# Performance work log

Hardware: AMD Instinct MI355X
Metric: run time of the kernel (lower is better)

Reference implementation:

```python
import jax, jax.numpy as jnp
import numpy as np

N = 50000
E = 800000
IN_F = 256
ATT_D = 256
H = 8
D_K = ATT_D // H  # 32
NORM_IDX = 0  # opt['attention_norm_idx']


def setup_inputs() -> dict:
    key = jax.random.key(0)
    ks = jax.random.split(key, 10)
    x = jax.random.normal(ks[0], (N, IN_F), dtype=jnp.float32)
    edge = jax.random.randint(ks[1], (2, E), 0, N, dtype=jnp.int64)
    edge_weights = jax.random.uniform(ks[2], (E,), dtype=jnp.float32)
    s = 0.02
    Wq = jax.random.normal(ks[3], (ATT_D, IN_F), dtype=jnp.float32) * s
    bq = jax.random.normal(ks[4], (ATT_D,), dtype=jnp.float32) * s
    Wk = jax.random.normal(ks[5], (ATT_D, IN_F), dtype=jnp.float32) * s
    bk = jax.random.normal(ks[6], (ATT_D,), dtype=jnp.float32) * s
    Wv = jax.random.normal(ks[7], (ATT_D, IN_F), dtype=jnp.float32) * s
    bv = jax.random.normal(ks[8], (ATT_D,), dtype=jnp.float32) * s
    return {"x": x, "edge": edge, "edge_weights": edge_weights,
            "Wq": Wq, "bq": bq, "Wk": Wk, "bk": bk, "Wv": Wv, "bv": bv}


def _segment_softmax(logits, seg, num_segments):
    # scatter-softmax grouped by seg (torch_geometric.utils.softmax semantics)
    m = jax.ops.segment_max(logits, seg, num_segments=num_segments)  # [N, H]
    ex = jnp.exp(logits - m[seg])
    s = jax.ops.segment_sum(ex, seg, num_segments=num_segments)
    return ex / (s[seg] + 1e-16)


def reference(x, edge, edge_weights, Wq, bq, Wk, bk, Wv, bv):
    # Linear projections, then [N, H, D_K] -> transpose to [N, D_K, H]
    q = (x @ Wq.T + bq).reshape(N, H, D_K).transpose(0, 2, 1)
    k = (x @ Wk.T + bk).reshape(N, H, D_K).transpose(0, 2, 1)
    v = (x @ Wv.T + bv).reshape(N, H, D_K).transpose(0, 2, 1)
    src = q[edge[0]]      # [E, D_K, H]
    dst_k = k[edge[1]]    # [E, D_K, H]
    prods = jnp.sum(src * dst_k, axis=1) / np.sqrt(D_K)  # [E, H]
    prods = prods * edge_weights[:, None]
    attention = _segment_softmax(prods, edge[NORM_IDX], N)  # [E, H]
    return attention, v
```

## Files before the change

kernel.cpp:

```cpp
#include <hip/hip_runtime.h>

#define NN 50000
#define EE 800000
#define FF 256
#define HH 8
#define DK 32

typedef short bf16x8 __attribute__((ext_vector_type(8)));
typedef float f32x4  __attribute__((ext_vector_type(4)));

__device__ __forceinline__ float b2f(short s) {
    return __uint_as_float(((unsigned)(unsigned short)s) << 16);
}
__device__ __forceinline__ short f2b(float f) {
    unsigned u = __float_as_uint(f);
    return (short)((u + 0x7fff + ((u >> 16) & 1)) >> 16);
}

__device__ __forceinline__ void gld16(void* lds, const void* g) {
    __builtin_amdgcn_global_load_lds(
        (const __attribute__((address_space(1))) unsigned int*)g,
        (__attribute__((address_space(3))) unsigned int*)lds,
        16, 0, 0);
}

__global__ __launch_bounds__(256) void sniff_all(
    const void* x, const void* ew, const void* wq, const void* bq,
    const void* wk, const void* bk, const void* wv, const void* bv,
    const void* edge, int* __restrict__ flags)
{
    __shared__ int tot;
    if (threadIdx.x == 0) tot = 0;
    __syncthreads();
    int b = blockIdx.x;
    if (b < 8) {
        const void* ptrs[8] = {x, ew, wq, bq, wk, bk, wv, bv};
        const int   ns[8]   = {NN * FF, EE, FF * FF, FF, FF * FF, FF, FF * FF, FF};
        const unsigned short* p = (const unsigned short*)ptrs[b];
        int half = ns[b] >> 1;
        int S = half < 4096 ? half : 4096;
        int cnt = 0;
        for (int i = threadIdx.x; i < S; i += 256) {
            unsigned v = p[2 * i];
            cnt += (((v >> 7) & 0xFF) >= 0xC0) ? 1 : 0;
        }
        atomicAdd(&tot, cnt);
        __syncthreads();
        if (threadIdx.x == 0) flags[b] = (tot * 32 > S) ? 1 : 0;
    } else {
        const unsigned* e32 = (const unsigned*)edge;
        int cnt = 0;
        for (int i = threadIdx.x; i < 4096; i += 256)
            cnt += (e32[2 * i + 1] != 0u) ? 1 : 0;
        atomicAdd(&tot, cnt);
        __syncthreads();
        if (threadIdx.x == 0) flags[8] = (tot < 100) ? 1 : 0;
    }
}

__global__ __launch_bounds__(256) void convert_wb(
    const void* wq, const void* wk, const void* wv,
    const void* bq, const void* bk, const void* bv,
    short* __restrict__ wb, float* __restrict__ bb,
    const int* __restrict__ flags)
{
    int b = blockIdx.x;
    if (b < 96) {
        int mat = b >> 5;
        const void* src = mat == 0 ? wq : mat == 1 ? wk : wv;
        int isf = flags[2 + mat * 2];
        int base = (b & 31) * 2048 + threadIdx.x * 8;
        bf16x8 v;
        if (isf) {
            const f32x4* pp = (const f32x4*)((const float*)src + base);
            f32x4 a = pp[0], c = pp[1];
            #pragma unroll
            for (int j = 0; j < 4; ++j) { v[j] = f2b(a[j]); v[4 + j] = f2b(c[j]); }
        } else {
            v = *(const bf16x8*)((const short*)src + base);
        }
        int row = base >> 8, k = base & 255;
        int s = k >> 5, quad = (k >> 3) & 3;
        int pc = (row << 2) + (quad ^ ((row >> 1) & 3));
        *(bf16x8*)(wb + mat * (FF * FF) + s * 8192 + pc * 8) = v;
    } else {
        #pragma unroll
        for (int mat = 0; mat < 3; ++mat) {
            const void* src = mat == 0 ? bq : mat == 1 ? bk : bv;
            int isf = flags[3 + mat * 2];
            int i = threadIdx.x;
            bb[mat * FF + i] = isf ? ((const float*)src)[i]
                                   : b2f(((const short*)src)[i]);
        }
    }
}

__global__ __launch_bounds__(256) void qkv_gemm(
    const void* __restrict__ x, const short* __restrict__ wb,
    const float* __restrict__ bb, short* __restrict__ qo,
    short* __restrict__ ko, float* __restrict__ vo,
    const int* __restrict__ flags, int ybase)
{
    __shared__ __align__(16) short wlds[2][8192];
    const int isf32x = flags[0];
    const int tid = threadIdx.x, wave = tid >> 6, lane = tid & 63;
    const int l16 = lane & 15, quad = lane >> 4;
    const int mat = ybase + blockIdx.y;
    const short* W = wb + mat * (FF * FF);
    const int rows0 = blockIdx.x * 64 + wave * 16;
    const int rowa = rows0 + l16;
    const int rowc = rowa < NN ? rowa : NN - 1;
    const int koff = quad * 8;
    const size_t xrow = (size_t)rowc * FF;

    const int rdo = l16 * 32 + ((quad ^ ((l16 >> 1) & 3)) << 3);

    f32x4 acc[16] = {};
    f32x4 ar0[2], ar1[2];
    bf16x8 ab[2];

    #define STAGE(buf, s) do {                                                  \
        const short* gs_ = W + (s) * 8192;                                      \
        _Pragma("unroll")                                                       \
        for (int i_ = 0; i_ < 4; ++i_)                                          \
            gld16(&wlds[buf][(i_ * 256 + (tid & ~63)) * 8],                     \
                  gs_ + (size_t)(i_ * 256 + tid) * 8);                          \
    } while (0)

    #define ALOAD(slot, s) do {                                                 \
        if (isf32x) {                                                           \
            const f32x4* p_ = (const f32x4*)((const float*)x + xrow + (s) * 32 + koff); \
            ar0[slot] = p_[0]; ar1[slot] = p_[1];                               \
        } else {                                                                \
            ab[slot] = *(const bf16x8*)((const short*)x + xrow + (s) * 32 + koff); \
        }                                                                       \
    } while (0)

    STAGE(0, 0);
    ALOAD(0, 0);
    __syncthreads();

    #pragma unroll
    for (int s = 0; s < 8; ++s) {
        const int cur = s & 1;
        if (s < 7) { STAGE(cur ^ 1, s + 1); ALOAD((s + 1) & 1, s + 1); }
        bf16x8 a;
        if (isf32x) {
            #pragma unroll
            for (int j = 0; j < 4; ++j) { a[j] = f2b(ar0[cur][j]); a[4 + j] = f2b(ar1[cur][j]); }
        } else {
            a = ab[cur];
        }
        const short* ws0 = &wlds[cur][rdo];
        #pragma unroll
        for (int c = 0; c < 16; ++c) {
            bf16x8 bf = *(const bf16x8*)(ws0 + c * 512);
            acc[c] = __builtin_amdgcn_mfma_f32_16x16x32_bf16(a, bf, acc[c], 0, 0, 0);
        }
        __syncthreads();
    }

    const float* bias = bb + mat * FF;
    short* slice = (short*)wlds + wave * 4096;

    if (mat == 2) {
        float* lsf = (float*)slice;
        #pragma unroll
        for (int h = 0; h < 2; ++h) {
            #pragma unroll
            for (int ci = 0; ci < 8; ++ci) {
                int c = ci * 2 + h;
                int col = c * 16 + l16;
                float bv = bias[col];
                int pcl = l16 * 8 + ci;
                #pragma unroll
                for (int rr = 0; rr < 4; ++rr)
                    lsf[(quad * 4 + rr) * 128 + pcl] = acc[c][rr] + bv;
            }
            #pragma unroll
            for (int it = 0; it < 8; ++it) {
                int idx = it * 64 + lane;
                int r = idx >> 5, cc = idx & 31;
                int row = rows0 + r;
                if (row < NN)
                    *(f32x4*)(vo + (size_t)row * FF + h * 128 + cc * 4) =
                        ((const f32x4*)lsf)[idx];
            }
        }
    } else {
        #pragma unroll
        for (int c = 0; c < 16; ++c) {
            int col = c * 16 + l16;
            float bv = bias[col];
            #pragma unroll
            for (int rr = 0; rr < 4; ++rr)
                slice[(quad * 4 + rr) * 256 + col] = f2b(acc[c][rr] + bv);
        }
        short* out = (mat == 0) ? qo : ko;
        #pragma unroll
        for (int it = 0; it < 8; ++it) {
            int idx = it * 64 + lane;
            int r = idx >> 5, cc = idx & 31;
            int row = rows0 + r;
            if (row < NN)
                *(bf16x8*)(out + (size_t)row * FF + cc * 8) =
                    *(const bf16x8*)(slice + r * 256 + cc * 8);
        }
    }
}

__device__ __forceinline__ float edge_exp_f(
    const int* __restrict__ edge, const void* __restrict__ ew,
    const short* __restrict__ q, const short* __restrict__ k,
    int t, int isf32, int is64, int* s_out)
{
    int e = t >> 3, h = t & 7;
    int s = is64 ? edge[2 * (size_t)e] : edge[e];
    int d = is64 ? edge[2 * ((size_t)EE + e)] : edge[EE + e];
    *s_out = s;
    const short* qp = q + (size_t)s * FF + h * DK;
    const short* kp = k + (size_t)d * FF + h * DK;
    float dot = 0.f;
    #pragma unroll
    for (int i = 0; i < 4; ++i) {
        bf16x8 qa = *(const bf16x8*)(qp + i * 8);
        bf16x8 ka = *(const bf16x8*)(kp + i * 8);
        #pragma unroll
        for (int j = 0; j < 8; ++j) dot += b2f(qa[j]) * b2f(ka[j]);
    }
    float w = isf32 ? ((const float*)ew)[e] : b2f(((const short*)ew)[e]);
    return __expf(dot * 0.17677669529663687f * w);
}

__global__ __launch_bounds__(256) void edge_pass_a(
    const int* __restrict__ edge, const void* __restrict__ ew,
    const short* __restrict__ q, const short* __restrict__ k,
    float* __restrict__ sums, float* __restrict__ expbuf,
    const int* __restrict__ flags, int use_exp)
{
    int t = blockIdx.x * 256 + threadIdx.x;
    int s;
    float exv = edge_exp_f(edge, ew, q, k, t, flags[1], flags[8], &s);
    if (use_exp) expbuf[t] = exv;
    atomicAdd(&sums[s * HH + (threadIdx.x & 7)], exv);
}

__global__ __launch_bounds__(256) void edge_pass_b(
    const int* __restrict__ edge, const void* __restrict__ ew,
    const short* __restrict__ q, const short* __restrict__ k,
    const float* __restrict__ sums, const float* __restrict__ expbuf,
    float* __restrict__ att, const int* __restrict__ flags, int use_exp)
{
    int t = blockIdx.x * 256 + threadIdx.x;
    float exv; int s;
    if (use_exp) {
        int e = t >> 3;
        s = flags[8] ? edge[2 * (size_t)e] : edge[e];
        exv = expbuf[t];
    } else {
        exv = edge_exp_f(edge, ew, q, k, t, flags[1], flags[8], &s);
    }
    att[t] = exv / (sums[s * HH + (t & 7)] + 1e-16f);
}

extern "C" void kernel_launch(void* const* d_in, const int* in_sizes, int n_in,
                              void* d_out, int out_size, void* d_ws, size_t ws_size,
                              hipStream_t stream) {
    const void* x    = d_in[0];
    const int*  edge = (const int*)d_in[1];
    const void* ew   = d_in[2];
    const void* Wq   = d_in[3];
    const void* bq   = d_in[4];
    const void* Wk   = d_in[5];
    const void* bk   = d_in[6];
    const void* Wv   = d_in[7];
    const void* bv   = d_in[8];

    float* att_out = (float*)d_out;
    float* v_out   = att_out + (size_t)EE * HH;

    char*  ws    = (char*)d_ws;
    int*   flags = (int*)ws;
    float* sums  = (float*)(ws + 256);
    const size_t SUMS_B = (size_t)NN * HH * 4;
    const size_t Q_B    = (size_t)NN * FF * 2;
    short* q_  = (short*)(ws + 256 + SUMS_B);
    short* wb  = (short*)(ws + 256 + SUMS_B + Q_B);
    float* bb  = (float*)(ws + 256 + SUMS_B + Q_B + 3 * FF * FF * 2);
    float* expb = (float*)(ws + 256 + SUMS_B + Q_B + 3 * FF * FF * 2 + 3 * FF * 4);
    const size_t BASE_B = 256 + SUMS_B + Q_B + 3 * FF * FF * 2 + 3 * FF * 4;
    const int use_exp = (ws_size >= BASE_B + (size_t)EE * HH * 4) ? 1 : 0;

    short* k_ = (short*)v_out;

    sniff_all<<<9, 256, 0, stream>>>(x, ew, Wq, bq, Wk, bk, Wv, bv, edge, flags);
    convert_wb<<<97, 256, 0, stream>>>(Wq, Wk, Wv, bq, bk, bv, wb, bb, flags);
    hipMemsetAsync(sums, 0, SUMS_B, stream);

    dim3 gqk((NN + 63) / 64, 2);
    qkv_gemm<<<gqk, 256, 0, stream>>>(x, wb, bb, q_, k_, nullptr, flags, 0);

    const int nEH = EE * HH;
    edge_pass_a<<<nEH / 256, 256, 0, stream>>>(edge, ew, q_, k_, sums, expb, flags, use_exp);
    edge_pass_b<<<nEH / 256, 256, 0, stream>>>(edge, ew, q_, k_, sums, expb, att_out, flags, use_exp);

    dim3 gv((NN + 63) / 64, 1);
    qkv_gemm<<<gv, 256, 0, stream>>>(x, wb, bb, nullptr, nullptr, v_out, flags, 2);
}
```

Measured before the change: 321.8 us.

## Fuse Q/K/V projections into one GEMM pass and precompute reciprocal softmax sums

The QKV GEMM now loads each block's x rows into registers once and loops over the weight matrices inside a single launch. It computes all three projections in one kernel when workspace allows, storing K in workspace instead of aliasing the V output. This removes the repeated x reads and the separate V GEMM launch, at the cost of more register pressure and less grid parallelism per launch. A small kernel also inverts the per-node softmax sums so the normalisation pass multiplies instead of divides, which adds one extra launch.

```diff
diff --git a/kernel.cpp b/kernel.cpp
--- a/kernel.cpp
+++ b/kernel.cpp
@@ -99,14 +99,12 @@
     const void* __restrict__ x, const short* __restrict__ wb,
     const float* __restrict__ bb, short* __restrict__ qo,
     short* __restrict__ ko, float* __restrict__ vo,
-    const int* __restrict__ flags, int ybase)
+    const int* __restrict__ flags, int mlo, int mhi)
 {
     __shared__ __align__(16) short wlds[2][8192];
     const int isf32x = flags[0];
     const int tid = threadIdx.x, wave = tid >> 6, lane = tid & 63;
     const int l16 = lane & 15, quad = lane >> 4;
-    const int mat = ybase + blockIdx.y;
-    const short* W = wb + mat * (FF * FF);
     const int rows0 = blockIdx.x * 64 + wave * 16;
     const int rowa = rows0 + l16;
     const int rowc = rowa < NN ? rowa : NN - 1;
@@ -115,98 +113,104 @@
 
     const int rdo = l16 * 32 + ((quad ^ ((l16 >> 1) & 3)) << 3);
 
-    f32x4 acc[16] = {};
-    f32x4 ar0[2], ar1[2];
-    bf16x8 ab[2];
-
-    #define STAGE(buf, s) do {                                                  \
-        const short* gs_ = W + (s) * 8192;                                      \
+    bf16x8 afrag[8];
+    if (isf32x) {
+        f32x4 t0[8], t1[8];
+        #pragma unroll
+        for (int s = 0; s < 8; ++s) {
+            const f32x4* p = (const f32x4*)((const float*)x + xrow + s * 32 + koff);
+            t0[s] = p[0]; t1[s] = p[1];
+        }
+        #pragma unroll
+        for (int s = 0; s < 8; ++s)
+            #pragma unroll
+            for (int j = 0; j < 4; ++j) {
+                afrag[s][j]     = f2b(t0[s][j]);
+                afrag[s][4 + j] = f2b(t1[s][j]);
+            }
+    } else {
+        #pragma unroll
+        for (int s = 0; s < 8; ++s)
+            afrag[s] = *(const bf16x8*)((const short*)x + xrow + s * 32 + koff);
+    }
+
+    #define STAGE(buf, W_, s) do {                                              \
+        const short* gs_ = (W_) + (s) * 8192;                                   \
         _Pragma("unroll")                                                       \
         for (int i_ = 0; i_ < 4; ++i_)                                          \
             gld16(&wlds[buf][(i_ * 256 + (tid & ~63)) * 8],                     \
                   gs_ + (size_t)(i_ * 256 + tid) * 8);                          \
     } while (0)
 
-    #define ALOAD(slot, s) do {                                                 \
-        if (isf32x) {                                                           \
-            const f32x4* p_ = (const f32x4*)((const float*)x + xrow + (s) * 32 + koff); \
-            ar0[slot] = p_[0]; ar1[slot] = p_[1];                               \
-        } else {                                                                \
-            ab[slot] = *(const bf16x8*)((const short*)x + xrow + (s) * 32 + koff); \
-        }                                                                       \
-    } while (0)
-
-    STAGE(0, 0);
-    ALOAD(0, 0);
-    __syncthreads();
-
-    #pragma unroll
-    for (int s = 0; s < 8; ++s) {
-        const int cur = s & 1;
-        if (s < 7) { STAGE(cur ^ 1, s + 1); ALOAD((s + 1) & 1, s + 1); }
-        bf16x8 a;
-        if (isf32x) {
-            #pragma unroll
-            for (int j = 0; j < 4; ++j) { a[j] = f2b(ar0[cur][j]); a[4 + j] = f2b(ar1[cur][j]); }
+    for (int mat = mlo; mat <= mhi; ++mat) {
+        const short* W = wb + mat * (FF * FF);
+        if (mat != mlo) __syncthreads();
+        STAGE(0, W, 0);
+        __syncthreads();
+
+        f32x4 acc[16] = {};
+        #pragma unroll
+        for (int s = 0; s < 8; ++s) {
+            const int cur = s & 1;
+            if (s < 7) STAGE(cur ^ 1, W, s + 1);
+            const short* ws0 = &wlds[cur][rdo];
+            #pragma unroll
+            for (int c = 0; c < 16; ++c) {
+                bf16x8 bf = *(const bf16x8*)(ws0 + c * 512);
+                acc[c] = __builtin_amdgcn_mfma_f32_16x16x32_bf16(afrag[s], bf, acc[c], 0, 0, 0);
+            }
+            __syncthreads();
+        }
+
+        const float* bias = bb + mat * FF;
+        short* slice = (short*)wlds + wave * 4096;
+
+        if (mat == 2) {
+            float* lsf = (float*)slice;
+            #pragma unroll
+            for (int h = 0; h < 2; ++h) {
+                #pragma unroll
+                for (int ci = 0; ci < 8; ++ci) {
+                    int c = ci * 2 + h;
+                    int col = c * 16 + l16;
+                    float bv = bias[col];
+                    int pcl = l16 * 8 + ci;
+                    #pragma unroll
+                    for (int rr = 0; rr < 4; ++rr)
+                        lsf[(quad * 4 + rr) * 128 + pcl] = acc[c][rr] + bv;
+                }
+                #pragma unroll
+                for (int it = 0; it < 8; ++it) {
+                    int idx = it * 64 + lane;
+                    int r = idx >> 5, cc = idx & 31;
+                    int row = rows0 + r;
+                    if (row < NN)
+                        *(f32x4*)(vo + (size_t)row * FF + h * 128 + cc * 4) =
+                            ((const f32x4*)lsf)[idx];
+                }
+            }
         } else {
-            a = ab[cur];
-        }
-        const short* ws0 = &wlds[cur][rdo];
-        #pragma unroll
-        for (int c = 0; c < 16; ++c) {
-            bf16x8 bf = *(const bf16x8*)(ws0 + c * 512);
-            acc[c] = __builtin_amdgcn_mfma_f32_16x16x32_bf16(a, bf, acc[c], 0, 0, 0);
-        }
-        __syncthreads();
-    }
-
-    const float* bias = bb + mat * FF;
-    short* slice = (short*)wlds + wave * 4096;
-
-    if (mat == 2) {
-        float* lsf = (float*)slice;
-        #pragma unroll
-        for (int h = 0; h < 2; ++h) {
-            #pragma unroll
-            for (int ci = 0; ci < 8; ++ci) {
-                int c = ci * 2 + h;
+            #pragma unroll
+            for (int c = 0; c < 16; ++c) {
                 int col = c * 16 + l16;
                 float bv = bias[col];
-                int pcl = l16 * 8 + ci;
                 #pragma unroll
                 for (int rr = 0; rr < 4; ++rr)
-                    lsf[(quad * 4 + rr) * 128 + pcl] = acc[c][rr] + bv;
-            }
+                    slice[(quad * 4 + rr) * 256 + col] = f2b(acc[c][rr] + bv);
+            }
+            short* out = (mat == 0) ? qo : ko;
             #pragma unroll
             for (int it = 0; it < 8; ++it) {
                 int idx = it * 64 + lane;
                 int r = idx >> 5, cc = idx & 31;
                 int row = rows0 + r;
                 if (row < NN)
-                    *(f32x4*)(vo + (size_t)row * FF + h * 128 + cc * 4) =
-                        ((const f32x4*)lsf)[idx];
-            }
-        }
-    } else {
-        #pragma unroll
-        for (int c = 0; c < 16; ++c) {
-            int col = c * 16 + l16;
-            float bv = bias[col];
-            #pragma unroll
-            for (int rr = 0; rr < 4; ++rr)
-                slice[(quad * 4 + rr) * 256 + col] = f2b(acc[c][rr] + bv);
-        }
-        short* out = (mat == 0) ? qo : ko;
-        #pragma unroll
-        for (int it = 0; it < 8; ++it) {
-            int idx = it * 64 + lane;
-            int r = idx >> 5, cc = idx & 31;
-            int row = rows0 + r;
-            if (row < NN)
-                *(bf16x8*)(out + (size_t)row * FF + cc * 8) =
-                    *(const bf16x8*)(slice + r * 256 + cc * 8);
-        }
-    }
+                    *(bf16x8*)(out + (size_t)row * FF + cc * 8) =
+                        *(const bf16x8*)(slice + r * 256 + cc * 8);
+            }
+        }
+    }
+    #undef STAGE
 }
 
 __device__ __forceinline__ float edge_exp_f(
@@ -245,6 +249,12 @@
     atomicAdd(&sums[s * HH + (threadIdx.x & 7)], exv);
 }
 
+__global__ __launch_bounds__(256) void rsum_inv(float* __restrict__ sums)
+{
+    int i = blockIdx.x * 256 + threadIdx.x;
+    if (i < NN * HH) sums[i] = 1.0f / (sums[i] + 1e-16f);
+}
+
 __global__ __launch_bounds__(256) void edge_pass_b(
     const int* __restrict__ edge, const void* __restrict__ ew,
     const short* __restrict__ q, const short* __restrict__ k,
@@ -260,7 +270,7 @@
     } else {
         exv = edge_exp_f(edge, ew, q, k, t, flags[1], flags[8], &s);
     }
-    att[t] = exv / (sums[s * HH + (t & 7)] + 1e-16f);
+    att[t] = exv * sums[s * HH + (t & 7)];
 }
 
 extern "C" void kernel_launch(void* const* d_in, const int* in_sizes, int n_in,
@@ -284,26 +294,34 @@
     float* sums  = (float*)(ws + 256);
     const size_t SUMS_B = (size_t)NN * HH * 4;
     const size_t Q_B    = (size_t)NN * FF * 2;
+    const size_t EXP_B  = (size_t)EE * HH * 4;
     short* q_  = (short*)(ws + 256 + SUMS_B);
     short* wb  = (short*)(ws + 256 + SUMS_B + Q_B);
     float* bb  = (float*)(ws + 256 + SUMS_B + Q_B + 3 * FF * FF * 2);
     float* expb = (float*)(ws + 256 + SUMS_B + Q_B + 3 * FF * FF * 2 + 3 * FF * 4);
     const size_t BASE_B = 256 + SUMS_B + Q_B + 3 * FF * FF * 2 + 3 * FF * 4;
-    const int use_exp = (ws_size >= BASE_B + (size_t)EE * HH * 4) ? 1 : 0;
-
-    short* k_ = (short*)v_out;
+    const int use_exp = (ws_size >= BASE_B + EXP_B) ? 1 : 0;
+    const int fused   = (ws_size >= BASE_B + EXP_B + Q_B) ? 1 : 0;
 
     sniff_all<<<9, 256, 0, stream>>>(x, ew, Wq, bq, Wk, bk, Wv, bv, edge, flags);
     convert_wb<<<97, 256, 0, stream>>>(Wq, Wk, Wv, bq, bk, bv, wb, bb, flags);
     hipMemsetAsync(sums, 0, SUMS_B, stream);
 
-    dim3 gqk((NN + 63) / 64, 2);
-    qkv_gemm<<<gqk, 256, 0, stream>>>(x, wb, bb, q_, k_, nullptr, flags, 0);
-
     const int nEH = EE * HH;
-    edge_pass_a<<<nEH / 256, 256, 0, stream>>>(edge, ew, q_, k_, sums, expb, flags, use_exp);
-    edge_pass_b<<<nEH / 256, 256, 0, stream>>>(edge, ew, q_, k_, sums, expb, att_out, flags, use_exp);
-
-    dim3 gv((NN + 63) / 64, 1);
-    qkv_gemm<<<gv, 256, 0, stream>>>(x, wb, bb, nullptr, nullptr, v_out, flags, 2);
-}
+    dim3 g((NN + 63) / 64);
+
+    if (fused) {
+        short* k_ = (short*)(ws + BASE_B + EXP_B);
+        qkv_gemm<<<g, 256, 0, stream>>>(x, wb, bb, q_, k_, v_out, flags, 0, 2);
+        edge_pass_a<<<nEH / 256, 256, 0, stream>>>(edge, ew, q_, k_, sums, expb, flags, 1);
+        rsum_inv<<<(NN * HH + 255) / 256, 256, 0, stream>>>(sums);
+        edge_pass_b<<<nEH / 256, 256, 0, stream>>>(edge, ew, q_, k_, sums, expb, att_out, flags, 1);
+    } else {
+        short* k_ = (short*)v_out;
+        qkv_gemm<<<g, 256, 0, stream>>>(x, wb, bb, q_, k_, nullptr, flags, 0, 1);
+        edge_pass_a<<<nEH / 256, 256, 0, stream>>>(edge, ew, q_, k_, sums, expb, flags, use_exp);
+        rsum_inv<<<(NN * HH + 255) / 256, 256, 0, stream>>>(sums);
+        edge_pass_b<<<nEH / 256, 256, 0, stream>>>(edge, ew, q_, k_, sums, expb, att_out, flags, use_exp);
+        qkv_gemm<<<g, 256, 0, stream>>>(x, wb, bb, nullptr, nullptr, v_out, flags, 2, 2);
+    }
+}
```

After: 336.7 us. +4.6%, slower.
